# Performance work log

Measured on AMD Instinct MI355X. Metric: run time of the kernel, lower is better.

The kernel has to match this reference:

```python
import jax, jax.numpy as jnp
import numpy as np


def setup_inputs() -> dict:
    key = jax.random.key(0)
    k1, k2, k3 = jax.random.split(key, 3)
    B, S, H, E = 8, 4096, 2048, 64
    hidden_states = jax.random.normal(k1, (B, S, H), dtype=jnp.float32)
    # kaiming_uniform-ish scale for the gate weight [E, H]
    weight = jax.random.normal(k2, (E, H), dtype=jnp.float32) * (1.0 / np.sqrt(H))
    # load-balancing biases are small perturbations of the softmax scores
    expert_biases = jax.random.normal(k3, (E,), dtype=jnp.float32) * 0.01
    return {"hidden_states": hidden_states, "weight": weight,
            "expert_biases": expert_biases, "top_k": 8}


def reference(hidden_states, weight, expert_biases, top_k):
    B, S, H = hidden_states.shape
    x = hidden_states.reshape(-1, H).astype(jnp.float32)          # [T, H], T = B*S
    logits = jnp.einsum('th,eh->te', x, weight.astype(jnp.float32))  # [T, E]
    scores = jax.nn.softmax(logits, axis=-1)                      # fp32 softmax
    bias_scores = scores + expert_biases[None, :]                 # bias-adjusted routing
    _, topk_indices = jax.lax.top_k(bias_scores, top_k)           # [T, K] (sorted; set equals torch sorted=False)
    topk_weights = jnp.take_along_axis(scores, topk_indices, axis=1)  # gather original probs
    if top_k > 1:  # norm_topk_prob=True
        topk_weights = topk_weights / (topk_weights.sum(-1, keepdims=True) + 1e-20)
    return (topk_indices.astype(jnp.int32),
            topk_weights.astype(hidden_states.dtype))
```

## Files before the change

### kernel.cpp

```cpp
#include <hip/hip_runtime.h>
#include <math.h>

#define Hdim   2048
#define HF4    512
#define MARGIN 2e-5f
#define CAPF   16384
#define PROBE0 1237
#define PROBE1 20011

#define WS_FCNT  0
#define WS_BAD   4
#define WS_PROBE 64
#define WS_FLIST 1024
#define WS_WH    (128*1024)
#define WS_WL    (384*1024)
#define WS_NEED  (640*1024)

typedef float f32x4 __attribute__((ext_vector_type(4)));
typedef short bf8   __attribute__((ext_vector_type(8)));

__device__ __forceinline__ short bf_hi(float v, float& rem) {
  const unsigned u  = __builtin_bit_cast(unsigned, v);
  const unsigned uh = u & 0xffff0000u;
  rem = v - __builtin_bit_cast(float, uh);
  return (short)(u >> 16);
}
__device__ __forceinline__ short bf_rne(float v) {
  const unsigned u = __builtin_bit_cast(unsigned, v);
  return (short)((u + 0x7fffu + ((u >> 16) & 1u)) >> 16);
}

__global__ __launch_bounds__(256) void gate_prep(
    const float* __restrict__ wgt, short* __restrict__ WH, short* __restrict__ WL)
{
  const int f  = blockIdx.x * 256 + threadIdx.x;
  const int c  = f >> 11;
  const int et = (f >> 9) & 3;
  const int l  = (f >> 3) & 63;
  const int j  = f & 7;
  const int e  = et * 16 + (l & 15);
  const int k  = c * 32 + (l >> 4) * 8 + j;
  const float w = wgt[(size_t)e * Hdim + k];
  float r; const short h = bf_hi(w, r);
  WH[f] = h; WL[f] = bf_rne(r);
}

__global__ __launch_bounds__(256, 2) void gate_main(
    const float* __restrict__ x, const short* __restrict__ WH,
    const short* __restrict__ WL, const float* __restrict__ eb,
    float* __restrict__ out, int* __restrict__ fcnt, int* __restrict__ flist,
    float* __restrict__ probelg, int T)
{
  const int t  = threadIdx.x;
  const int wv = t >> 6;
  const int ln = t & 63;
  const int tb = blockIdx.x * 64 + wv * 16;

  const char* xq = (const char*)(x + (size_t)(tb + (ln & 15)) * Hdim + (ln >> 4) * 8);
  const short* whp = WH;
  const short* wlp = WL;
  const unsigned voff = (unsigned)(ln * 16);

  f32x4 acc[4];
  #pragma unroll
  for (int et = 0; et < 4; ++et) acc[et] = (f32x4)0.f;

  f32x4 P0a, P0b, P1a, P1b, P2a, P2b, P3a, P3b;
  bf8 WEh0, WEh1, WEh2, WEh3, WEl0, WEl1, WEl2, WEl3;
  bf8 WOh0, WOh1, WOh2, WOh3, WOl0, WOl1, WOl2, WOl3;

#define XLOAD(D0, D1, OA, OB)                                              \
  asm volatile("global_load_dwordx4 %0, %2, off offset:" #OA "\n\t"        \
               "global_load_dwordx4 %1, %2, off offset:" #OB               \
               : "=v"(D0), "=v"(D1) : "v"(xq))

#define WLOAD(H0,H1,H2,H3,L0,L1,L2,L3)                                     \
  asm volatile(                                                            \
    "global_load_dwordx4 %0, %8, %9  offset:0\n\t"                         \
    "global_load_dwordx4 %1, %8, %9  offset:1024\n\t"                      \
    "global_load_dwordx4 %2, %8, %9  offset:2048\n\t"                      \
    "global_load_dwordx4 %3, %8, %9  offset:3072\n\t"                      \
    "global_load_dwordx4 %4, %8, %10 offset:0\n\t"                         \
    "global_load_dwordx4 %5, %8, %10 offset:1024\n\t"                      \
    "global_load_dwordx4 %6, %8, %10 offset:2048\n\t"                      \
    "global_load_dwordx4 %7, %8, %10 offset:3072"                          \
    : "=v"(H0), "=v"(H1), "=v"(H2), "=v"(H3),                              \
      "=v"(L0), "=v"(L1), "=v"(L2), "=v"(L3)                               \
    : "v"(voff), "s"(whp), "s"(wlp));                                      \
  whp += 2048; wlp += 2048;

#define WAITC(VM)                                                          \
  asm volatile("s_waitcnt vmcnt(" #VM ")" ::: "memory");                   \
  __builtin_amdgcn_sched_barrier(0);

#define COMP(XA, XB, H0,H1,H2,H3, L0,L1,L2,L3) {                                  \
    bf8 ah, al;                                                                   \
    _Pragma("unroll")                                                             \
    for (int j = 0; j < 4; ++j) { float r_;                                       \
      ah[j]     = bf_hi(XA[j], r_);  al[j]     = bf_rne(r_);                      \
      ah[j + 4] = bf_hi(XB[j], r_);  al[j + 4] = bf_rne(r_); }                    \
    __builtin_amdgcn_s_setprio(1);                                                \
    acc[0] = __builtin_amdgcn_mfma_f32_16x16x32_bf16(ah, H0, acc[0], 0, 0, 0);    \
    acc[0] = __builtin_amdgcn_mfma_f32_16x16x32_bf16(ah, L0, acc[0], 0, 0, 0);    \
    acc[0] = __builtin_amdgcn_mfma_f32_16x16x32_bf16(al, H0, acc[0], 0, 0, 0);    \
    acc[0] = __builtin_amdgcn_mfma_f32_16x16x32_bf16(al, L0, acc[0], 0, 0, 0);    \
    acc[1] = __builtin_amdgcn_mfma_f32_16x16x32_bf16(ah, H1, acc[1], 0, 0, 0);    \
    acc[1] = __builtin_amdgcn_mfma_f32_16x16x32_bf16(ah, L1, acc[1], 0, 0, 0);    \
    acc[1] = __builtin_amdgcn_mfma_f32_16x16x32_bf16(al, H1, acc[1], 0, 0, 0);    \
    acc[1] = __builtin_amdgcn_mfma_f32_16x16x32_bf16(al, L1, acc[1], 0, 0, 0);    \
    acc[2] = __builtin_amdgcn_mfma_f32_16x16x32_bf16(ah, H2, acc[2], 0, 0, 0);    \
    acc[2] = __builtin_amdgcn_mfma_f32_16x16x32_bf16(ah, L2, acc[2], 0, 0, 0);    \
    acc[2] = __builtin_amdgcn_mfma_f32_16x16x32_bf16(al, H2, acc[2], 0, 0, 0);    \
    acc[2] = __builtin_amdgcn_mfma_f32_16x16x32_bf16(al, L2, acc[2], 0, 0, 0);    \
    acc[3] = __builtin_amdgcn_mfma_f32_16x16x32_bf16(ah, H3, acc[3], 0, 0, 0);    \
    acc[3] = __builtin_amdgcn_mfma_f32_16x16x32_bf16(ah, L3, acc[3], 0, 0, 0);    \
    acc[3] = __builtin_amdgcn_mfma_f32_16x16x32_bf16(al, H3, acc[3], 0, 0, 0);    \
    acc[3] = __builtin_amdgcn_mfma_f32_16x16x32_bf16(al, L3, acc[3], 0, 0, 0);    \
    __builtin_amdgcn_s_setprio(0);                                                \
  }

#define CE(XA,XB) COMP(XA,XB, WEh0,WEh1,WEh2,WEh3, WEl0,WEl1,WEl2,WEl3)
#define CO(XA,XB) COMP(XA,XB, WOh0,WOh1,WOh2,WOh3, WOl0,WOl1,WOl2,WOl3)
#define WE_ WLOAD(WEh0,WEh1,WEh2,WEh3, WEl0,WEl1,WEl2,WEl3)
#define WO_ WLOAD(WOh0,WOh1,WOh2,WOh3, WOl0,WOl1,WOl2,WOl3)

  WE_;
  XLOAD(P0a, P0b, 0, 16);
  WO_;
  XLOAD(P1a, P1b, 128, 144);
  XLOAD(P2a, P2b, 256, 272);

  #pragma unroll 1
  for (int it = 0; it < 15; ++it) {
    WAITC(12); CE(P0a, P0b); WE_; XLOAD(P3a, P3b, 384, 400);
    WAITC(12); CO(P1a, P1b); WO_; XLOAD(P0a, P0b, 512, 528);
    WAITC(12); CE(P2a, P2b); WE_; XLOAD(P1a, P1b, 640, 656);
    WAITC(12); CO(P3a, P3b); WO_; XLOAD(P2a, P2b, 768, 784);
    xq += 512;
  }
  WAITC(12); CE(P0a, P0b); WE_; XLOAD(P3a, P3b, 384, 400);
  WAITC(12); CO(P1a, P1b); WO_;
  WAITC(10); CE(P2a, P2b);
  WAITC(0);  CO(P3a, P3b);
#undef WE_
#undef WO_
#undef CE
#undef CO
#undef COMP
#undef WAITC
#undef WLOAD
#undef XLOAD

  const int c = ln & 15, g = ln >> 4;
  float bias4[4];
  #pragma unroll
  for (int et = 0; et < 4; ++et) bias4[et] = eb[et * 16 + c];

  #pragma unroll
  for (int r = 0; r < 4; ++r) {
    const int gt = tb + g * 4 + r;
    const float z0 = acc[0][r], z1 = acc[1][r], z2 = acc[2][r], z3 = acc[3][r];
    if (gt == PROBE0) { probelg[c]      = z0; probelg[16 + c] = z1;
                        probelg[32 + c] = z2; probelg[48 + c] = z3; }
    if (gt == PROBE1) { probelg[64 + c]  = z0; probelg[80 + c]  = z1;
                        probelg[96 + c]  = z2; probelg[112 + c] = z3; }
    float m = fmaxf(fmaxf(z0, z1), fmaxf(z2, z3));
    #pragma unroll
    for (int off = 1; off < 16; off <<= 1) m = fmaxf(m, __shfl_xor(m, off, 64));
    const float p0 = expf(z0 - m), p1 = expf(z1 - m);
    const float p2 = expf(z2 - m), p3 = expf(z3 - m);
    float Zs = (p0 + p1) + (p2 + p3);
    #pragma unroll
    for (int off = 1; off < 16; off <<= 1) Zs += __shfl_xor(Zs, off, 64);
    const float inv = 1.f / Zs;
    const float s0 = p0 * inv, s1 = p1 * inv, s2 = p2 * inv, s3 = p3 * inv;
    float b0 = s0 + bias4[0], b1 = s1 + bias4[1];
    float b2 = s2 + bias4[2], b3 = s3 + bias4[3];
    float prev = 0.f, gmin = 1e30f, mys = 0.f;
    int myi = 0;
    #pragma unroll
    for (int r9 = 0; r9 < 9; ++r9) {
      float v = b0; int ie = 0;
      if (b1 > v) { v = b1; ie = 1; }
      if (b2 > v) { v = b2; ie = 2; }
      if (b3 > v) { v = b3; ie = 3; }
      int idx = ie * 16 + c;
      #pragma unroll
      for (int off = 1; off < 16; off <<= 1) {
        const float ov = __shfl_xor(v, off, 64);
        const int   oi = __shfl_xor(idx, off, 64);
        if (ov > v || (ov == v && oi < idx)) { v = ov; idx = oi; }
      }
      if (r9) gmin = fminf(gmin, prev - v);
      prev = v;
      if (r9 < 8) {
        const int oe = idx >> 4, oc = idx & 15;
        const float cand = oe == 0 ? s0 : oe == 1 ? s1 : oe == 2 ? s2 : s3;
        const float sv = __shfl(cand, g * 16 + oc, 64);
        if (c == r9) { myi = idx; mys = sv; }
        if (c == oc) {
          if (oe == 0) b0 = -1e30f;
          else if (oe == 1) b1 = -1e30f;
          else if (oe == 2) b2 = -1e30f;
          else b3 = -1e30f;
        }
      }
    }
    float wsum = (c < 8) ? mys : 0.f;
    #pragma unroll
    for (int off = 1; off < 16; off <<= 1) wsum += __shfl_xor(wsum, off, 64);
    if (c < 8) {
      out[(size_t)gt * 8 + c] = (float)myi;
      out[(size_t)T * 8 + (size_t)gt * 8 + c] = mys / (wsum + 1e-20f);
    }
    if (c == 0 && gmin < MARGIN) {
      const int pos = atomicAdd(fcnt, 1);
      if (pos < CAPF) flist[pos] = gt;
    }
  }
}

__global__ __launch_bounds__(256) void gate_check(
    const float* __restrict__ x, const float* __restrict__ wgt,
    const float* __restrict__ probelg, const int* __restrict__ fcnt,
    int* __restrict__ allbad)
{
  __shared__ float part[64][4];
  const int p = blockIdx.x;
  const int P = p ? PROBE1 : PROBE0;
  const int t = threadIdx.x, e = t >> 2, q = t & 3;
  const float4* xr = (const float4*)(x + (size_t)P * Hdim);
  const float4* wr = (const float4*)(wgt + (size_t)e * Hdim);
  float a = 0.f, b = 0.f, c = 0.f, d = 0.f;
  for (int i = 0; i < 128; ++i) {
    const int f4 = i * 4 + q;
    const float4 xv = xr[f4], wv = wr[f4];
    a = fmaf(xv.x, wv.x, a); b = fmaf(xv.y, wv.y, b);
    c = fmaf(xv.z, wv.z, c); d = fmaf(xv.w, wv.w, d);
  }
  part[e][q] = (a + b) + (c + d);
  __syncthreads();
  if (q == 0) {
    const float z = part[e][0] + part[e][1] + part[e][2] + part[e][3];
    if (fabsf(z - probelg[p * 64 + e]) > 0.05f) *allbad = 1;
  }
  if (t == 0 && p == 0 && *fcnt > CAPF) *allbad = 1;
}

__global__ __launch_bounds__(256) void gate_fix(
    const float* __restrict__ x, const float* __restrict__ wgt,
    const float* __restrict__ eb, float* __restrict__ out,
    const int* __restrict__ fcnt, const int* __restrict__ flist,
    const int* __restrict__ allbad, int T)
{
  __shared__ float4 xl[4 * HF4];
  __shared__ double part[4][64][4];
  __shared__ int tks[4];
  const int bad = *allbad;
  int n = bad ? T : *fcnt;
  if (n <= 0) return;
  if (!bad && n > CAPF) n = CAPF;
  const int nb = (n + 3) >> 2;
  const int t = threadIdx.x;
  for (int b = blockIdx.x; b < nb; b += gridDim.x) {
    if (t < 4) {
      const int li = b * 4 + t;
      const int ci = li < n ? li : n - 1;
      tks[t] = bad ? ci : flist[ci];
    }
    __syncthreads();
    {
      const int m = t >> 6, l2 = t & 63;
      const float4* src = (const float4*)x + (size_t)tks[m] * HF4;
      #pragma unroll
      for (int ii = 0; ii < 8; ++ii) xl[m * HF4 + ii * 64 + l2] = src[ii * 64 + l2];
    }
    __syncthreads();
    const int e = t >> 2, q = t & 3;
    double acc[4] = {0.0, 0.0, 0.0, 0.0};
    const float4* w4 = (const float4*)wgt + (size_t)e * HF4;
    for (int c = 0; c < 128; ++c) {
      const int f4 = c * 4 + q;
      const float4 wvv = w4[f4];
      #pragma unroll
      for (int m = 0; m < 4; ++m) {
        const float4 xv = xl[m * HF4 + f4];
        acc[m] += (double)xv.x * (double)wvv.x + (double)xv.y * (double)wvv.y
                + (double)xv.z * (double)wvv.z + (double)xv.w * (double)wvv.w;
      }
    }
    #pragma unroll
    for (int m = 0; m < 4; ++m) part[m][e][q] = acc[m];
    __syncthreads();
    {
      const int m = t >> 6, ln = t & 63;
      const double z = part[m][ln][0] + part[m][ln][1] + part[m][ln][2] + part[m][ln][3];
      double mx = z;
      #pragma unroll
      for (int off = 32; off; off >>= 1) mx = fmax(mx, __shfl_xor(mx, off, 64));
      const double p = exp(z - mx);
      double Zs = p;
      #pragma unroll
      for (int off = 32; off; off >>= 1) Zs += __shfl_xor(Zs, off, 64);
      const double sco = p / Zs;
      double bsw = sco + (double)eb[ln];
      double mys = 0.0;
      int myi = 0;
      #pragma unroll
      for (int r = 0; r < 8; ++r) {
        double v = bsw;
        int idx = ln;
        #pragma unroll
        for (int off = 32; off; off >>= 1) {
          const double ov = __shfl_xor(v, off, 64);
          const int   oi = __shfl_xor(idx, off, 64);
          if (ov > v || (ov == v && oi < idx)) { v = ov; idx = oi; }
        }
        const double sv = __shfl(sco, idx, 64);
        if (ln == r)  { myi = idx; mys = sv; }
        if (ln == idx) bsw = -1.0e300;
      }
      double wsum = (ln < 8) ? mys : 0.0;
      #pragma unroll
      for (int off = 32; off; off >>= 1) wsum += __shfl_xor(wsum, off, 64);
      const int gt = tks[m];
      if (ln < 8) {
        out[(size_t)gt * 8 + ln] = (float)myi;
        out[(size_t)T * 8 + (size_t)gt * 8 + ln] = (float)(mys / (wsum + 1e-20));
      }
    }
    __syncthreads();
  }
}

extern "C" void kernel_launch(void* const* d_in, const int* in_sizes, int n_in,
                              void* d_out, int out_size, void* d_ws, size_t ws_size,
                              hipStream_t stream) {
  const float* x   = (const float*)d_in[0];
  const float* wgt = (const float*)d_in[1];
  const float* eb  = (const float*)d_in[2];
  float* out = (float*)d_out;
  const int T = in_sizes[0] / Hdim;
  char* ws = (char*)d_ws;
  int*   fcnt    = (int*)(ws + WS_FCNT);
  int*   bad     = (int*)(ws + WS_BAD);
  float* probelg = (float*)(ws + WS_PROBE);
  int*   flist   = (int*)(ws + WS_FLIST);
  short* WH      = (short*)(ws + WS_WH);
  short* WL      = (short*)(ws + WS_WL);

  if (ws_size < WS_NEED) {
    hipMemsetAsync(ws, 0, 8, stream);
    hipMemsetAsync(ws + WS_BAD, 1, 1, stream);
    hipLaunchKernelGGL(gate_fix, dim3(256), dim3(256), 0, stream,
                       x, wgt, eb, out, fcnt, flist, bad, T);
    return;
  }
  hipMemsetAsync(ws, 0, 8, stream);
  hipLaunchKernelGGL(gate_prep, dim3(512), dim3(256), 0, stream, wgt, WH, WL);
  hipLaunchKernelGGL(gate_main, dim3(T / 64), dim3(256), 0, stream,
                     x, WH, WL, eb, out, fcnt, flist, probelg, T);
  hipLaunchKernelGGL(gate_check, dim3(2), dim3(256), 0, stream,
                     x, wgt, probelg, fcnt, bad);
  hipLaunchKernelGGL(gate_fix, dim3(256), dim3(256), 0, stream,
                     x, wgt, eb, out, fcnt, flist, bad, T);
}
```

Before: 166.8 us.

## Split K dimension across wave pairs with LDS reduction in gate_main

```diff
diff --git a/kernel.cpp b/kernel.cpp
--- a/kernel.cpp
+++ b/kernel.cpp
@@ -45,27 +45,31 @@
   WH[f] = h; WL[f] = bf_rne(r);
 }
 
-__global__ __launch_bounds__(256, 2) void gate_main(
+__global__ __launch_bounds__(256, 3) void gate_main(
     const float* __restrict__ x, const short* __restrict__ WH,
     const short* __restrict__ WL, const float* __restrict__ eb,
     float* __restrict__ out, int* __restrict__ fcnt, int* __restrict__ flist,
     float* __restrict__ probelg, int T)
 {
+  __shared__ float redu[2][64][17];
   const int t  = threadIdx.x;
   const int wv = t >> 6;
+  const int tg = wv >> 1;
+  const int kh = wv & 1;
   const int ln = t & 63;
-  const int tb = blockIdx.x * 64 + wv * 16;
-
-  const char* xq = (const char*)(x + (size_t)(tb + (ln & 15)) * Hdim + (ln >> 4) * 8);
+  const int tb = blockIdx.x * 32 + tg * 16;
+
+  const char* xq = (const char*)(x + (size_t)(tb + (ln & 15)) * Hdim
+                                 + (size_t)kh * 1024 + (ln >> 4) * 8);
   const short* whp = WH;
   const short* wlp = WL;
-  const unsigned voff = (unsigned)(ln * 16);
+  const unsigned voff = (unsigned)(ln * 16) + ((unsigned)kh << 17);
 
   f32x4 acc[4];
   #pragma unroll
   for (int et = 0; et < 4; ++et) acc[et] = (f32x4)0.f;
 
-  f32x4 P0a, P0b, P1a, P1b, P2a, P2b, P3a, P3b;
+  f32x4 P0a, P0b, P1a, P1b;
   bf8 WEh0, WEh1, WEh2, WEh3, WEl0, WEl1, WEl2, WEl3;
   bf8 WOh0, WOh1, WOh2, WOh3, WOl0, WOl1, WOl2, WOl3;
 
@@ -74,20 +78,19 @@
                "global_load_dwordx4 %1, %2, off offset:" #OB               \
                : "=v"(D0), "=v"(D1) : "v"(xq))
 
-#define WLOAD(H0,H1,H2,H3,L0,L1,L2,L3)                                     \
+#define WLOAD4(D0,D1,D2,D3, BASE)                                          \
   asm volatile(                                                            \
-    "global_load_dwordx4 %0, %8, %9  offset:0\n\t"                         \
-    "global_load_dwordx4 %1, %8, %9  offset:1024\n\t"                      \
-    "global_load_dwordx4 %2, %8, %9  offset:2048\n\t"                      \
-    "global_load_dwordx4 %3, %8, %9  offset:3072\n\t"                      \
-    "global_load_dwordx4 %4, %8, %10 offset:0\n\t"                         \
-    "global_load_dwordx4 %5, %8, %10 offset:1024\n\t"                      \
-    "global_load_dwordx4 %6, %8, %10 offset:2048\n\t"                      \
-    "global_load_dwordx4 %7, %8, %10 offset:3072"                          \
-    : "=v"(H0), "=v"(H1), "=v"(H2), "=v"(H3),                              \
-      "=v"(L0), "=v"(L1), "=v"(L2), "=v"(L3)                               \
-    : "v"(voff), "s"(whp), "s"(wlp));                                      \
-  whp += 2048; wlp += 2048;
+    "global_load_dwordx4 %0, %4, %5 offset:0\n\t"                          \
+    "global_load_dwordx4 %1, %4, %5 offset:1024\n\t"                       \
+    "global_load_dwordx4 %2, %4, %5 offset:2048\n\t"                       \
+    "global_load_dwordx4 %3, %4, %5 offset:3072"                           \
+    : "=v"(D0), "=v"(D1), "=v"(D2), "=v"(D3)                               \
+    : "v"(voff), "s"(BASE))
+
+#define WSTG(H0,H1,H2,H3, L0,L1,L2,L3) {                                   \
+    WLOAD4(H0,H1,H2,H3, whp);                                              \
+    WLOAD4(L0,L1,L2,L3, wlp);                                              \
+    whp += 2048; wlp += 2048; }
 
 #define WAITC(VM)                                                          \
   asm volatile("s_waitcnt vmcnt(" #VM ")" ::: "memory");                   \
@@ -121,35 +124,48 @@
 
 #define CE(XA,XB) COMP(XA,XB, WEh0,WEh1,WEh2,WEh3, WEl0,WEl1,WEl2,WEl3)
 #define CO(XA,XB) COMP(XA,XB, WOh0,WOh1,WOh2,WOh3, WOl0,WOl1,WOl2,WOl3)
-#define WE_ WLOAD(WEh0,WEh1,WEh2,WEh3, WEl0,WEl1,WEl2,WEl3)
-#define WO_ WLOAD(WOh0,WOh1,WOh2,WOh3, WOl0,WOl1,WOl2,WOl3)
-
-  WE_;
-  XLOAD(P0a, P0b, 0, 16);
-  WO_;
-  XLOAD(P1a, P1b, 128, 144);
-  XLOAD(P2a, P2b, 256, 272);
+#define WE_ WSTG(WEh0,WEh1,WEh2,WEh3, WEl0,WEl1,WEl2,WEl3)
+#define WO_ WSTG(WOh0,WOh1,WOh2,WOh3, WOl0,WOl1,WOl2,WOl3)
+
+  WE_;  XLOAD(P0a, P0b, 0,   16);
+  WO_;  XLOAD(P1a, P1b, 128, 144);
 
   #pragma unroll 1
-  for (int it = 0; it < 15; ++it) {
-    WAITC(12); CE(P0a, P0b); WE_; XLOAD(P3a, P3b, 384, 400);
-    WAITC(12); CO(P1a, P1b); WO_; XLOAD(P0a, P0b, 512, 528);
-    WAITC(12); CE(P2a, P2b); WE_; XLOAD(P1a, P1b, 640, 656);
-    WAITC(12); CO(P3a, P3b); WO_; XLOAD(P2a, P2b, 768, 784);
+  for (int it = 0; it < 7; ++it) {
+    WAITC(10); CE(P0a, P0b); WE_; XLOAD(P0a, P0b, 256, 272);
+    WAITC(10); CO(P1a, P1b); WO_; XLOAD(P1a, P1b, 384, 400);
+    WAITC(10); CE(P0a, P0b); WE_; XLOAD(P0a, P0b, 512, 528);
+    WAITC(10); CO(P1a, P1b); WO_; XLOAD(P1a, P1b, 640, 656);
     xq += 512;
   }
-  WAITC(12); CE(P0a, P0b); WE_; XLOAD(P3a, P3b, 384, 400);
-  WAITC(12); CO(P1a, P1b); WO_;
-  WAITC(10); CE(P2a, P2b);
-  WAITC(0);  CO(P3a, P3b);
+  WAITC(10); CE(P0a, P0b); WE_; XLOAD(P0a, P0b, 256, 272);
+  WAITC(10); CO(P1a, P1b); WO_; XLOAD(P1a, P1b, 384, 400);
+  WAITC(10); CE(P0a, P0b);
+  WAITC(0);  CO(P1a, P1b);
 #undef WE_
 #undef WO_
 #undef CE
 #undef CO
 #undef COMP
 #undef WAITC
-#undef WLOAD
+#undef WSTG
+#undef WLOAD4
 #undef XLOAD
+
+  if (kh) {
+    #pragma unroll
+    for (int et = 0; et < 4; ++et)
+      #pragma unroll
+      for (int r = 0; r < 4; ++r)
+        redu[tg][ln][et * 4 + r] = acc[et][r];
+  }
+  __syncthreads();
+  if (kh) return;
+  #pragma unroll
+  for (int et = 0; et < 4; ++et)
+    #pragma unroll
+    for (int r = 0; r < 4; ++r)
+      acc[et][r] += redu[tg][ln][et * 4 + r];
 
   const int c = ln & 15, g = ln >> 4;
   float bias4[4];
@@ -350,15 +366,15 @@
   short* WL      = (short*)(ws + WS_WL);
 
   if (ws_size < WS_NEED) {
-    hipMemsetAsync(ws, 0, 8, stream);
-    hipMemsetAsync(ws + WS_BAD, 1, 1, stream);
+    (void)hipMemsetAsync(ws, 0, 8, stream);
+    (void)hipMemsetAsync(ws + WS_BAD, 1, 1, stream);
     hipLaunchKernelGGL(gate_fix, dim3(256), dim3(256), 0, stream,
                        x, wgt, eb, out, fcnt, flist, bad, T);
     return;
   }
-  hipMemsetAsync(ws, 0, 8, stream);
+  (void)hipMemsetAsync(ws, 0, 8, stream);
   hipLaunchKernelGGL(gate_prep, dim3(512), dim3(256), 0, stream, wgt, WH, WL);
-  hipLaunchKernelGGL(gate_main, dim3(T / 64), dim3(256), 0, stream,
+  hipLaunchKernelGGL(gate_main, dim3(T / 32), dim3(256), 0, stream,
                      x, WH, WL, eb, out, fcnt, flist, probelg, T);
   hipLaunchKernelGGL(gate_check, dim3(2), dim3(256), 0, stream,
                      x, wgt, probelg, fcnt, bad);
```

Measured after the change: 166.9 us. Within noise of the previous version (+0.1%).
